# Optimization experiments

Hardware: AMD Instinct MI355X
Metric: run time of the kernel (lower is better)

Reference implementation:

```python
import jax, jax.numpy as jnp
import numpy as np

KSIZE, STRIDE, SCALE = 7, 4, 10.0


def _same_pad_amounts(n, k, s):
    out = -(-n // s)
    pad = max(0, (out - 1) * s + k - n)
    return pad // 2, pad - pad // 2, out


def _conv(x, w, b, stride=1, pad=0):
    y = jax.lax.conv_general_dilated(
        x, w, (stride, stride), [(pad, pad), (pad, pad)],
        dimension_numbers=("NCHW", "OIHW", "NCHW"))
    return y + b[None, :, None, None]


def setup_inputs() -> dict:
    key = jax.random.key(0)
    ks = jax.random.split(key, 10)
    B, Cin, H, W = 2, 64, 256, 256
    Ci = 16                       # inter_channels
    d_in = KSIZE * KSIZE * Ci     # 784 = ksize^2 * inter_channels
    d_out = d_in // 4             # 196
    s = 0.02
    return {
        "b": jax.random.normal(ks[0], (B, Cin, H, W), jnp.float32),
        "g_w": jax.random.normal(ks[1], (Ci, Cin, 3, 3), jnp.float32) * s,
        "g_b": jnp.zeros((Ci,), jnp.float32),
        "theta_w": jax.random.normal(ks[2], (Ci, Cin, 1, 1), jnp.float32) * s,
        "theta_b": jnp.zeros((Ci,), jnp.float32),
        "W_w": jax.random.normal(ks[3], (Cin, Ci, 1, 1), jnp.float32) * s,
        "W_b": jnp.zeros((Cin,), jnp.float32),
        "fc1_w": jax.random.normal(ks[4], (d_out, d_in), jnp.float32) * s,
        "fc1_b": jnp.zeros((d_out,), jnp.float32),
        "fc2_w": jax.random.normal(ks[5], (d_out, d_in), jnp.float32) * s,
        "fc2_b": jnp.zeros((d_out,), jnp.float32),
        "thr_w": jax.random.normal(ks[6], (1, Cin, KSIZE, KSIZE), jnp.float32) * s,
        "thr_b": jnp.zeros((1,), jnp.float32),
        "bias_w": jax.random.normal(ks[7], (1, Cin, KSIZE, KSIZE), jnp.float32) * s,
        "bias_b": jnp.zeros((1,), jnp.float32),
    }


def _forward(b, g_w, g_b, theta_w, theta_b, W_w, W_b, fc1_w, fc1_b,
             fc2_w, fc2_b, thr_w, thr_b, bias_w, bias_b):
    B, Cin, H, W = b.shape
    k, s = KSIZE, STRIDE
    pt, pb, Lh = _same_pad_amounts(H, k, s)
    pl, pr, Lw = _same_pad_amounts(W, k, s)
    L = Lh * Lw
    Ci = g_w.shape[0]

    b1 = _conv(b, g_w, g_b, 1, 1)            # [B,Ci,H,W]
    b2 = _conv(b, theta_w, theta_b, 1, 0)    # [B,Ci,H,W]
    b4 = jnp.pad(b, ((0, 0), (0, 0), (pt, pb), (pl, pr)))
    thr = _conv(b4, thr_w, thr_b, s, 0).reshape(B, L)   # per-patch threshold
    bias = _conv(b4, bias_w, bias_b, s, 0).reshape(B, L)  # per-patch bias

    # patch gather indices on the 'same'-padded grid (torch.Unfold order)
    R = (jnp.arange(Lh) * s)[:, None] + jnp.arange(k)[None, :]   # [Lh,k]
    Cc = (jnp.arange(Lw) * s)[:, None] + jnp.arange(k)[None, :]  # [Lw,k]
    Ri = R[:, None, :, None]                                     # -> [Lh,Lw,k,k]
    Cj = Cc[None, :, None, :]

    def patches(x):  # [B,Ci,H,W] -> [B,L,Ci*k*k], flatten order (C,kh,kw)
        xp = jnp.pad(x, ((0, 0), (0, 0), (pt, pb), (pl, pr)))
        p = xp[:, :, Ri, Cj]                       # [B,Ci,Lh,Lw,k,k]
        return p.transpose(0, 2, 3, 1, 4, 5).reshape(B, L, -1)

    wi = patches(b1)     # stride_1 patches of b1
    xi = wi              # b3 = b1 and stride_1 == stride_2 -> identical patches
    pi = patches(b2)     # stride_2 patches of b2, values to aggregate

    wi_f = jax.nn.relu(jnp.einsum("bld,od->blo", wi, fc1_w) + fc1_b)
    xi_f = jax.nn.relu(jnp.einsum("bld,od->blo", xi, fc2_w) + fc2_b)
    score = jnp.einsum("blo,bmo->blm", wi_f, xi_f)   # [B,L,L] patch similarity

    # threshold-gated sparse attention with learned per-patch thr/bias
    mask = (score >= thr[:, :, None]).astype(score.dtype)
    gated = score * mask + bias[:, :, None]
    attn = jax.nn.softmax(gated * SCALE, axis=-1) * mask
    attn = attn / (attn.sum(-1, keepdims=True) + 1e-8)

    agg = jnp.einsum("blm,bmd->bld", attn, pi)       # [B,L,Ci*k*k]
    p6 = agg.reshape(B, Lh, Lw, Ci, k, k).transpose(0, 3, 1, 2, 4, 5)

    # fold back (sum overlaps), normalize by overlap count, crop padding
    Hp, Wp = H + pt + pb, W + pl + pr
    folded = jnp.zeros((B, Ci, Hp, Wp), score.dtype).at[:, :, Ri, Cj].add(p6)
    cnt = jnp.zeros((Hp, Wp), score.dtype).at[Ri, Cj].add(1.0)
    zi = (folded / cnt)[:, :, pl:pl + H, pt:pt + W]

    return b + _conv(zi, W_w, W_b, 1, 0)


def reference(b, g_w, g_b, theta_w, theta_b, W_w, W_b, fc1_w, fc1_b,
              fc2_w, fc2_b, thr_w, thr_b, bias_w, bias_b):
    return _forward(b, g_w, g_b, theta_w, theta_b, W_w, W_b, fc1_w, fc1_b,
                    fc2_w, fc2_b, thr_w, thr_b, bias_w, bias_b)
```

## Files before the change

kernel.cpp:

```cpp
#include <hip/hip_runtime.h>
#include <math.h>

#define CIN  64
#define CI   16
#define HH   256
#define WWD  256
#define KS   7
#define STR  4
#define LH   64
#define LWD  64
#define LL   4096
#define DIN  784
#define DINP 896
#define DKP  832
#define DOUT 196
#define DOUTP 256
#define NB   2
#define YP   258
#define XP   264

typedef __attribute__((ext_vector_type(8))) short bf16x8;
typedef __attribute__((ext_vector_type(4))) float f32x4;
typedef __attribute__((ext_vector_type(16))) float f32x16;
typedef __attribute__((ext_vector_type(8))) int i32x8;
typedef __attribute__((ext_vector_type(4))) int i32x4;

__device__ __forceinline__ unsigned short f2bf(float x) {
    unsigned int u = __float_as_uint(x);
    unsigned int r = (u + 0x7FFFu + ((u >> 16) & 1u)) >> 16;
    return (unsigned short)r;
}
__device__ __forceinline__ float bf2f(unsigned short h) {
    return __uint_as_float(((unsigned int)h) << 16);
}

__device__ __forceinline__ void stage16(const void* g, void* l) {
#if defined(__has_builtin)
#if __has_builtin(__builtin_amdgcn_global_load_lds)
    __builtin_amdgcn_global_load_lds(
        (const __attribute__((address_space(1))) unsigned int*)g,
        (__attribute__((address_space(3))) unsigned int*)l, 16, 0, 0);
    return;
#endif
#endif
    *(float4*)l = *(const float4*)g;
}

__global__ __launch_bounds__(256) void k_prep_b(const float* __restrict__ b,
                                                unsigned short* __restrict__ bTp) {
    int blk = blockIdx.x;
    int s = blk & 7; int yy = (blk >> 3) % YP; int n = blk / (8 * YP);
    int y = yy - 1;
    for (int xx = threadIdx.x; xx < XP; xx += 256) {
        int x = xx - 4;
        bool v = (y >= 0 && y < 256 && x >= 0 && x < 256);
        unsigned short h[8];
#pragma unroll
        for (int j = 0; j < 8; j++)
            h[j] = v ? f2bf(b[((size_t)(n * 64 + s * 8 + j) * 256 + y) * 256 + x]) : (unsigned short)0;
        *(uint4*)&bTp[((((size_t)n * YP + yy) * 8 + s) * XP + xx) * 8] = *(uint4*)h;
    }
}

__global__ void k_prep_wb(const float* __restrict__ g_w, const float* __restrict__ th_w,
                          unsigned short* __restrict__ wbt) {
    int i = blockIdx.x * 256 + threadIdx.x;
    if (i >= 18432) return;
    int j = i & 7, co = (i >> 3) & 31, q = (i >> 8) & 3, h = (i >> 10) & 1, t = i >> 11;
    int ci = h * 32 + q * 8 + j;
    float v;
    if (co < 16) v = g_w[((size_t)co * 64 + ci) * 9 + t];
    else         v = (t == 4) ? th_w[(size_t)(co - 16) * 64 + ci] : 0.f;
    wbt[i] = f2bf(v);
}

__global__ void k_prep_fc(const float* __restrict__ fc1_w, const float* __restrict__ fc2_w,
                          unsigned short* __restrict__ fcwb) {
    int i = blockIdx.x * 256 + threadIdx.x;
    if (i >= 2 * DOUTP * DKP) return;
    int col = i % DKP; int row = (i / DKP) % DOUTP; int f = i / (DKP * DOUTP);
    float v = 0.f;
    if (row < DOUT && col < DIN) v = (f ? fc2_w : fc1_w)[row * DIN + col];
    fcwb[i] = f2bf(v);
}

__global__ __launch_bounds__(256) void k_convm(
        const unsigned short* __restrict__ bTp, const unsigned short* __restrict__ wbt,
        const float* __restrict__ g_b, const float* __restrict__ th_b,
        unsigned short* __restrict__ bx) {
    __shared__ unsigned short wb[18432];
    __shared__ unsigned short ti[8 * 3 * 68 * 8];
    int tid = threadIdx.x;
#pragma unroll
    for (int i = 0; i < 9; i++) {
        int c = i * 256 + tid;
        stage16(wbt + (size_t)c * 8, &wb[c * 8]);
    }
    int n = blockIdx.x >> 8, y = blockIdx.x & 255;
    int wave = tid >> 6, lane = tid & 63, lr = lane & 15, q = lane >> 4;
    int m0 = wave * 16;
    float bg = g_b[lr], bt = th_b[lr];
    for (int xs = 0; xs < 4; xs++) {
        __syncthreads();
        int x0 = xs * 64;
#pragma unroll
        for (int i = 0; i < 7; i++) {
            int c = i * 256 + tid;
            if (c < 1632) {
                int s = c / 204; int rem = c % 204; int r = rem / 68; int cc = rem % 68;
                const unsigned short* src =
                    bTp + ((((size_t)n * YP + y + r) * 8 + s) * XP + (x0 + 3 + cc)) * 8;
                stage16(src, &ti[c * 8]);
            }
        }
        __syncthreads();
        f32x4 a0 = {bg, bg, bg, bg}, a1 = {bt, bt, bt, bt};
#pragma unroll
        for (int t = 0; t < 9; t++) {
            int dy = t / 3, dx = t % 3;
#pragma unroll
            for (int h = 0; h < 2; h++) {
                int s = h * 4 + q;
                bf16x8 av = *(const bf16x8*)&ti[(((s * 3 + dy) * 68) + m0 + lr + dx) * 8];
                bf16x8 b0 = *(const bf16x8*)&wb[((((t * 2 + h) * 4 + q) * 32) + lr) * 8];
                bf16x8 b1 = *(const bf16x8*)&wb[((((t * 2 + h) * 4 + q) * 32) + 16 + lr) * 8];
                a0 = __builtin_amdgcn_mfma_f32_16x16x32_bf16(av, b0, a0, 0, 0, 0);
                a1 = __builtin_amdgcn_mfma_f32_16x16x32_bf16(av, b1, a1, 0, 0, 0);
            }
        }
        size_t pb = (((size_t)n * 256 + y) * 256 + x0 + m0 + q * 4);
#pragma unroll
        for (int r = 0; r < 4; r++) {
            bx[(pb + r) * 32 + lr]      = f2bf(a0[r]);
            bx[(pb + r) * 32 + 16 + lr] = f2bf(a1[r]);
        }
    }
}

__global__ __launch_bounds__(256) void k_thr(
        const unsigned short* __restrict__ bTp, const float* __restrict__ thr_w,
        const float* __restrict__ thr_b, float* __restrict__ thr) {
    __shared__ float w[64 * 49];
    int tid = threadIdx.x;
    for (int i = tid; i < 64 * 49; i += 256) w[i] = thr_w[i];
    __syncthreads();
    int wid = (blockIdx.x << 2) + (tid >> 6);
    int lane = tid & 63;
    int s = lane >> 3, j = lane & 7;
    int n = wid >> 12, l = wid & 4095;
    int lh = (l >> 6), lw = l & 63;
    const float* wl = w + (s * 8 + j) * 49;
    float acc = 0.f;
#pragma unroll
    for (int dy = 0; dy < 7; dy++) {
        int yy = lh * 4 + dy;
        if (yy >= YP) continue;
        const unsigned short* row = bTp + (((size_t)(n * YP + yy) * 8 + s) * XP) * 8;
#pragma unroll
        for (int dx = 0; dx < 7; dx++) {
            int xx = lw * 4 + dx + 3;
            acc = fmaf(bf2f(row[xx * 8 + j]), wl[dy * 7 + dx], acc);
        }
    }
#pragma unroll
    for (int off = 32; off > 0; off >>= 1) acc += __shfl_down(acc, off, 64);
    if (lane == 0) thr[wid] = acc + thr_b[0];
}

__global__ void k_patchesA(const unsigned short* __restrict__ bx, unsigned short* __restrict__ Pb) {
    size_t e = (size_t)blockIdx.x * 256 + threadIdx.x;
    if (e >= (size_t)NB * LL * DKP) return;
    int d = (int)(e % DKP); size_t r = e / DKP;
    int l = (int)(r & 4095); int n = (int)(r >> 12);
    unsigned short v = 0;
    if (d < DIN) {
        int ci = d / 49; int t = d % 49; int dy = t / 7; int dx = t % 7;
        int y = (l >> 6) * 4 + dy - 1, x = (l & 63) * 4 + dx - 1;
        if (y >= 0 && y < 256 && x >= 0 && x < 256)
            v = bx[(((size_t)n * 256 + y) * 256 + x) * 32 + ci];
    }
    Pb[e] = v;
}

__global__ void k_patchesT(const unsigned short* __restrict__ bx, unsigned char* __restrict__ piT8) {
    size_t e = (size_t)blockIdx.x * 256 + threadIdx.x;
    int l = (int)(e & 4095);
    int d = (int)((e >> 12) % DINP);
    int n = (int)(e / ((size_t)DINP * LL));
    float v = 0.f;
    if (d < DIN) {
        int ci = d / 49; int t = d % 49; int dy = t / 7; int dx = t % 7;
        int y = (l >> 6) * 4 + dy - 1, x = (l & 63) * 4 + dx - 1;
        if (y >= 0 && y < 256 && x >= 0 && x < 256)
            v = bf2f(bx[(((size_t)n * 256 + y) * 256 + x) * 32 + 16 + ci]);
    }
    int p = __builtin_amdgcn_cvt_pk_fp8_f32(v, 0.f, 0, false);
    piT8[e] = (unsigned char)(p & 0xFF);
}

template<int MODE>
__global__ __launch_bounds__(256) void k_gemm_nt(
        const unsigned short* __restrict__ A, const unsigned short* __restrict__ Bt,
        void* __restrict__ C, int lda, int ldb, int ldc, int K,
        size_t sA, size_t sB, size_t sC,
        const float* __restrict__ bias1, const float* __restrict__ bias2) {
    __shared__ unsigned short lA[2][128 * 64];
    __shared__ unsigned short lB[2][128 * 64];
    int tid = threadIdx.x;
    int wave = tid >> 6, lane = tid & 63;
    int lr = lane & 15, lq = lane >> 4;
    int wm = (wave >> 1) * 64, wn = (wave & 1) * 64;
    int i0 = blockIdx.x * 128, j0 = blockIdx.y * 128;
    int z = blockIdx.z;
    int az = (MODE == 2) ? (z >> 1) : z;
    int bz = (MODE == 2) ? (z & 1) : z;
    const unsigned short* Ab = A + (size_t)az * sA + (size_t)i0 * lda;
    const unsigned short* Bb = Bt + (size_t)bz * sB + (size_t)j0 * ldb;

    auto stageAB = [&](int buf, int k0) {
#pragma unroll
        for (int it = 0; it < 4; it++) {
            int c = it * 256 + tid;
            int row = c >> 3, slot = c & 7;
            int col8 = slot ^ (row & 7);
            stage16(Ab + (size_t)row * lda + k0 + col8 * 8, &lA[buf][c * 8]);
        }
#pragma unroll
        for (int it = 0; it < 4; it++) {
            int c = it * 256 + tid;
            int row = c >> 3, slot = c & 7;
            int col8 = slot ^ (row & 7);
            stage16(Bb + (size_t)row * ldb + k0 + col8 * 8, &lB[buf][c * 8]);
        }
    };

    f32x4 acc[4][4] = {};
    int NT = K >> 6;
    stageAB(0, 0);
    stageAB(1, 64);
    for (int t = 0; t < NT; ++t) {
        int cur = t & 1;
        if (t + 1 < NT) { asm volatile("s_waitcnt vmcnt(8)" ::: "memory"); }
        else            { asm volatile("s_waitcnt vmcnt(0)" ::: "memory"); }
        __builtin_amdgcn_s_barrier();
#pragma unroll
        for (int ks = 0; ks < 2; ks++) {
            bf16x8 af[4], bfr[4];
#pragma unroll
            for (int t2 = 0; t2 < 4; t2++) {
                int row = wm + t2 * 16 + lr;
                int slot = ks * 4 + lq;
                af[t2] = *(const bf16x8*)&lA[cur][row * 64 + (slot ^ (row & 7)) * 8];
            }
#pragma unroll
            for (int t2 = 0; t2 < 4; t2++) {
                int row = wn + t2 * 16 + lr;
                int slot = ks * 4 + lq;
                bfr[t2] = *(const bf16x8*)&lB[cur][row * 64 + (slot ^ (row & 7)) * 8];
            }
#pragma unroll
            for (int mi = 0; mi < 4; mi++)
#pragma unroll
                for (int nj = 0; nj < 4; nj++)
                    acc[mi][nj] = __builtin_amdgcn_mfma_f32_16x16x32_bf16(
                        af[mi], bfr[nj], acc[mi][nj], 0, 0, 0);
        }
        asm volatile("s_waitcnt lgkmcnt(0)" ::: "memory");
        __builtin_amdgcn_s_barrier();
        if (t + 2 < NT) stageAB(cur, (t + 2) << 6);
    }
    if (MODE == 1) {
        unsigned short* Cb = (unsigned short*)C + (size_t)z * sC;
#pragma unroll
        for (int mi = 0; mi < 4; mi++)
#pragma unroll
            for (int r = 0; r < 4; r++) {
                int row = i0 + wm + mi * 16 + lq * 4 + r;
#pragma unroll
                for (int nj = 0; nj < 4; nj++)
                    Cb[(size_t)row * ldc + j0 + wn + nj * 16 + lr] = f2bf(acc[mi][nj][r]);
            }
    } else {
        const float* biasp = bz ? bias2 : bias1;
        unsigned short* Cb = (unsigned short*)C + (size_t)z * sC;
#pragma unroll
        for (int mi = 0; mi < 4; mi++)
#pragma unroll
            for (int r = 0; r < 4; r++) {
                int row = i0 + wm + mi * 16 + lq * 4 + r;
#pragma unroll
                for (int nj = 0; nj < 4; nj++) {
                    int col = j0 + wn + nj * 16 + lr;
                    float bv = (col < DOUT) ? biasp[col] : 0.f;
                    float v = fmaxf(acc[mi][nj][r] + bv, 0.f);
                    Cb[(size_t)row * ldc + col] = f2bf(v);
                }
            }
    }
}

__global__ __launch_bounds__(256) void k_gemm_mx(
        const unsigned char* __restrict__ A, const unsigned char* __restrict__ Bt,
        unsigned short* __restrict__ C, int lda, int ldb, int ldc, int K,
        size_t sA, size_t sB, size_t sC) {
    __shared__ unsigned char lA[2][128 * 128];
    __shared__ unsigned char lB[2][128 * 128];
    int tid = threadIdx.x;
    int wave = tid >> 6, lane = tid & 63;
    int lr = lane & 31, hf = lane >> 5;
    int wm = (wave >> 1) * 64, wn = (wave & 1) * 64;
    int i0 = blockIdx.x * 128, j0 = blockIdx.y * 128;
    int z = blockIdx.z;
    const unsigned char* Ab = A + (size_t)z * sA + (size_t)i0 * lda;
    const unsigned char* Bb = Bt + (size_t)z * sB + (size_t)j0 * ldb;

    auto stageAB = [&](int buf, int k0) {
#pragma unroll
        for (int it = 0; it < 4; it++) {
            int c = it * 256 + tid;
            int row = c >> 3, slot = c & 7;
            int col16 = slot ^ ((row ^ (row >> 3)) & 7);
            stage16(Ab + (size_t)row * lda + k0 + col16 * 16, &lA[buf][c * 16]);
        }
#pragma unroll
        for (int it = 0; it < 4; it++) {
            int c = it * 256 + tid;
            int row = c >> 3, slot = c & 7;
            int col16 = slot ^ ((row ^ (row >> 3)) & 7);
            stage16(Bb + (size_t)row * ldb + k0 + col16 * 16, &lB[buf][c * 16]);
        }
    };

    f32x16 acc[2][2] = {};
    int NT = K >> 7;
    stageAB(0, 0);
    stageAB(1, 128);
    for (int t = 0; t < NT; ++t) {
        int cur = t & 1;
        if (t + 1 < NT) { asm volatile("s_waitcnt vmcnt(8)" ::: "memory"); }
        else           { asm volatile("s_waitcnt vmcnt(0)" ::: "memory"); }
        __builtin_amdgcn_s_barrier();
        asm volatile("" ::: "memory");
#pragma unroll
        for (int kk = 0; kk < 2; kk++) {
            i32x8 af[2], bfv[2];
            int c0 = kk * 4 + hf * 2;
#pragma unroll
            for (int t2 = 0; t2 < 2; t2++) {
                int row = wm + t2 * 32 + lr;
                int sw = (row ^ (row >> 3)) & 7;
                i32x4 lo = *(const i32x4*)&lA[cur][row * 128 + ((c0    ) ^ sw) * 16];
                i32x4 hi = *(const i32x4*)&lA[cur][row * 128 + ((c0 + 1) ^ sw) * 16];
                af[t2][0] = lo[0]; af[t2][1] = lo[1]; af[t2][2] = lo[2]; af[t2][3] = lo[3];
                af[t2][4] = hi[0]; af[t2][5] = hi[1]; af[t2][6] = hi[2]; af[t2][7] = hi[3];
            }
#pragma unroll
            for (int t2 = 0; t2 < 2; t2++) {
                int row = wn + t2 * 32 + lr;
                int sw = (row ^ (row >> 3)) & 7;
                i32x4 lo = *(const i32x4*)&lB[cur][row * 128 + ((c0    ) ^ sw) * 16];
                i32x4 hi = *(const i32x4*)&lB[cur][row * 128 + ((c0 + 1) ^ sw) * 16];
                bfv[t2][0] = lo[0]; bfv[t2][1] = lo[1]; bfv[t2][2] = lo[2]; bfv[t2][3] = lo[3];
                bfv[t2][4] = hi[0]; bfv[t2][5] = hi[1]; bfv[t2][6] = hi[2]; bfv[t2][7] = hi[3];
            }
#pragma unroll
            for (int mi = 0; mi < 2; mi++)
#pragma unroll
                for (int nj = 0; nj < 2; nj++)
                    acc[mi][nj] = __builtin_amdgcn_mfma_scale_f32_32x32x64_f8f6f4(
                        af[mi], bfv[nj], acc[mi][nj],
                        0, 0,
                        0, 0x7F7F7F7F,
                        0, 0x7F7F7F7F);
        }
        asm volatile("s_waitcnt lgkmcnt(0)" ::: "memory");
        __builtin_amdgcn_s_barrier();
        if (t + 2 < NT) stageAB(cur, (t + 2) << 7);
    }
    unsigned short* Cb = C + (size_t)z * sC;
#pragma unroll
    for (int mi = 0; mi < 2; mi++)
#pragma unroll
        for (int nj = 0; nj < 2; nj++)
#pragma unroll
            for (int reg = 0; reg < 16; reg++) {
                int row = i0 + wm + mi * 32 + (reg & 3) + 8 * (reg >> 2) + 4 * hf;
                int col = j0 + wn + nj * 32 + lr;
                Cb[(size_t)row * ldc + col] = f2bf(acc[mi][nj][reg]);
            }
}

__global__ __launch_bounds__(256) void k_softmax(
        const unsigned short* __restrict__ score, const float* __restrict__ thr,
        unsigned char* __restrict__ attn8) {
    __shared__ float red[256], red2[256];
    int row = blockIdx.x, tid = threadIdx.x;
    const uint4* g4 = (const uint4*)(score + (size_t)row * LL);
    float t = thr[row];
    uint4 u0 = g4[tid], u1 = g4[tid + 256];
    float v[16];
    {
        unsigned int w[8] = {u0.x, u0.y, u0.z, u0.w, u1.x, u1.y, u1.z, u1.w};
#pragma unroll
        for (int q = 0; q < 8; q++) {
            v[2 * q]     = __uint_as_float(w[q] << 16);
            v[2 * q + 1] = __uint_as_float(w[q] & 0xFFFF0000u);
        }
    }
    float mx = 0.f;
#pragma unroll
    for (int k = 0; k < 16; k++) if (v[k] >= t) mx = fmaxf(mx, v[k]);
    red[tid] = mx; __syncthreads();
    for (int st = 128; st > 0; st >>= 1) {
        if (tid < st) red[tid] = fmaxf(red[tid], red[tid + st]);
        __syncthreads();
    }
    float M = 10.f * fmaxf(red[0], 0.f);
    __syncthreads();
    float e[16];
    float s2 = 0.f, n0 = 0.f;
#pragma unroll
    for (int k = 0; k < 16; k++) {
        if (v[k] >= t) { e[k] = __expf(10.f * v[k] - M); s2 += e[k]; }
        else           { e[k] = 0.f; n0 += 1.f; }
    }
    red[tid] = s2; red2[tid] = n0; __syncthreads();
    for (int st = 128; st > 0; st >>= 1) {
        if (tid < st) { red[tid] += red[tid + st]; red2[tid] += red2[tid + st]; }
        __syncthreads();
    }
    float S2 = red[0], N0 = red2[0];
    float iD = 1.f / (S2 + 1e-8f * (S2 + N0 * __expf(-M)));
#pragma unroll
    for (int i = 0; i < 2; i++) {
        int c = tid + i * 256;
        int d0 = __builtin_amdgcn_cvt_pk_fp8_f32(e[i * 8 + 0] * iD, e[i * 8 + 1] * iD, 0, false);
        d0     = __builtin_amdgcn_cvt_pk_fp8_f32(e[i * 8 + 2] * iD, e[i * 8 + 3] * iD, d0, true);
        int d1 = __builtin_amdgcn_cvt_pk_fp8_f32(e[i * 8 + 4] * iD, e[i * 8 + 5] * iD, 0, false);
        d1     = __builtin_amdgcn_cvt_pk_fp8_f32(e[i * 8 + 6] * iD, e[i * 8 + 7] * iD, d1, true);
        *(uint2*)&attn8[(size_t)row * LL + (size_t)c * 8] = make_uint2((unsigned)d0, (unsigned)d1);
    }
}

__global__ void k_fold(const unsigned short* __restrict__ aggb, float* __restrict__ zi) {
    int p = blockIdx.x * 256 + threadIdx.x;
    int x = p & 255, y = (p >> 8) & 255, ci = (p >> 16) & 15, n = p >> 20;
    int yp = y + 1, xp = x + 1;
    int lh1 = yp >> 2; if (lh1 > 63) lh1 = 63;
    int lh0 = (yp >= 3) ? ((yp - 3) >> 2) : 0;
    int lw1 = xp >> 2; if (lw1 > 63) lw1 = 63;
    int lw0 = (xp >= 3) ? ((xp - 3) >> 2) : 0;
    const unsigned short* a0 = aggb + (size_t)n * LL * DINP;
    float sum = 0.f;
    for (int lh = lh0; lh <= lh1; lh++) {
        int dy = yp - 4 * lh;
        for (int lw = lw0; lw <= lw1; lw++) {
            int dx = xp - 4 * lw;
            sum += bf2f(a0[(size_t)(lh * 64 + lw) * DINP + ci * 49 + dy * 7 + dx]);
        }
    }
    float cnt = (float)((lh1 - lh0 + 1) * (lw1 - lw0 + 1));
    zi[p] = sum / cnt;
}

__global__ void k_final(const float* __restrict__ zi, const float* __restrict__ b,
                        const float* __restrict__ W_w, const float* __restrict__ W_b,
                        float* __restrict__ out) {
    __shared__ float w[16 * 64];
    int tid = threadIdx.x;
    for (int i = tid; i < 16 * 64; i += 256) {
        int ci = i >> 6; int co = i & 63;
        w[i] = W_w[co * 16 + ci];
    }
    __syncthreads();
    int p = blockIdx.x * 256 + tid;
    int n = p >> 16, yx = p & 65535;
    float acc[64];
#pragma unroll
    for (int co = 0; co < 64; co++) acc[co] = 0.f;
    const float* zn = zi + (size_t)n * 16 * 65536;
#pragma unroll
    for (int ci = 0; ci < 16; ci++) {
        float v = zn[ci * 65536 + yx];
#pragma unroll
        for (int co = 0; co < 64; co++) acc[co] += v * w[ci * 64 + co];
    }
    const float* bn = b + (size_t)n * 64 * 65536;
    float* on = out + (size_t)n * 64 * 65536;
#pragma unroll
    for (int co = 0; co < 64; co++) on[co * 65536 + yx] = bn[co * 65536 + yx] + acc[co] + W_b[co];
}

extern "C" void kernel_launch(void* const* d_in, const int* in_sizes, int n_in,
                              void* d_out, int out_size, void* d_ws, size_t ws_size,
                              hipStream_t stream) {
    const float* b     = (const float*)d_in[0];
    const float* g_w   = (const float*)d_in[1];
    const float* g_b   = (const float*)d_in[2];
    const float* th_w  = (const float*)d_in[3];
    const float* th_b  = (const float*)d_in[4];
    const float* W_w   = (const float*)d_in[5];
    const float* W_b   = (const float*)d_in[6];
    const float* fc1_w = (const float*)d_in[7];
    const float* fc1_b = (const float*)d_in[8];
    const float* fc2_w = (const float*)d_in[9];
    const float* fc2_b = (const float*)d_in[10];
    const float* thr_w = (const float*)d_in[11];
    const float* thr_b = (const float*)d_in[12];
    float* out = (float*)d_out;

    float* ws = (float*)d_ws;
    size_t off = 0;
    auto alloc = [&](size_t nf) { float* p = ws + off; off += (nf + 63) & ~(size_t)63; return p; };
    unsigned short* aggb = (unsigned short*)alloc((size_t)NB * LL * DINP / 2);
    float* zi   = alloc((size_t)NB * CI * HH * WWD);
    unsigned short* bTp  = (unsigned short*)alloc((size_t)NB * YP * 8 * XP * 8 / 2);
    unsigned short* bx   = (unsigned short*)alloc((size_t)NB * HH * WWD * 32 / 2);
    unsigned short* Pb   = (unsigned short*)alloc((size_t)NB * LL * DKP / 2);
    unsigned char*  piT8 = (unsigned char*)alloc((size_t)NB * DINP * LL / 4);
    unsigned short* fcout = (unsigned short*)alloc((size_t)NB * 2 * LL * DOUTP / 2);
    unsigned short* wbt  = (unsigned short*)alloc(18432 / 2);
    unsigned short* fcwb = (unsigned short*)alloc((size_t)2 * DOUTP * DKP / 2);
    float* thr  = alloc((size_t)NB * LL);
    unsigned short* score = (unsigned short*)alloc((size_t)NB * LL * LL / 2);
    unsigned char*  attn8 = (unsigned char*)alloc((size_t)NB * LL * LL / 4);

    k_prep_b<<<dim3(NB * YP * 8), 256, 0, stream>>>(b, bTp);
    k_prep_wb<<<dim3(72), 256, 0, stream>>>(g_w, th_w, wbt);
    k_prep_fc<<<dim3((2 * DOUTP * DKP + 255) / 256), 256, 0, stream>>>(fc1_w, fc2_w, fcwb);
    k_convm<<<dim3(NB * 256), 256, 0, stream>>>(bTp, wbt, g_b, th_b, bx);
    k_thr<<<dim3(2048), 256, 0, stream>>>(bTp, thr_w, thr_b, thr);
    k_patchesA<<<dim3((int)((size_t)NB * LL * DKP / 256)), 256, 0, stream>>>(bx, Pb);
    k_patchesT<<<dim3((int)((size_t)NB * DINP * LL / 256)), 256, 0, stream>>>(bx, piT8);
    k_gemm_nt<2><<<dim3(32, 2, 4), 256, 0, stream>>>(
        Pb, fcwb, (void*)fcout, DKP, DKP, DOUTP, DKP,
        (size_t)LL * DKP, (size_t)DOUTP * DKP, (size_t)LL * DOUTP, fc1_b, fc2_b);
    k_gemm_nt<1><<<dim3(32, 32, NB), 256, 0, stream>>>(
        fcout, fcout + (size_t)LL * DOUTP, (void*)score, DOUTP, DOUTP, LL, DOUTP,
        (size_t)2 * LL * DOUTP, (size_t)2 * LL * DOUTP, (size_t)LL * LL, nullptr, nullptr);
    k_softmax<<<dim3(NB * LL), 256, 0, stream>>>(score, thr, attn8);
    k_gemm_mx<<<dim3(32, DINP / 128, NB), 256, 0, stream>>>(
        attn8, piT8, aggb, LL, LL, DINP, LL,
        (size_t)LL * LL, (size_t)DINP * LL, (size_t)LL * DINP);
    k_fold<<<dim3(8192), 256, 0, stream>>>(aggb, zi);
    k_final<<<dim3(512), 256, 0, stream>>>(zi, b, W_w, W_b, out);
}
```

Before: 323.0 us.

## Fuse patch extraction into one LDS-staged kernel and XCD-swizzle GEMM grids

Merges the two element-wise patch-extraction kernels into one kernel. It stages a 7x68 pixel tile of the conv output in shared memory and writes both the bf16 patch matrix and the transposed fp8 patch matrix with 16-byte vector stores. This removes redundant scattered global gathers and byte-wide stores. Separately, the GEMM launches become 1D grids remapped so that consecutive tiles land on the same XCD (stride-8 interleave), aiming for better L2 reuse across chiplets. The remap assumes the block count is divisible by 8.

```diff
diff --git a/kernel.cpp b/kernel.cpp
--- a/kernel.cpp
+++ b/kernel.cpp
@@ -46,6 +46,13 @@
     *(float4*)l = *(const float4*)g;
 }
 
+__device__ __forceinline__ void swz_grid(int gx, int gy, int& ib, int& jb, int& zb) {
+    int total = gridDim.x;
+    int flat = blockIdx.x;
+    int s = (flat & 7) * (total >> 3) + (flat >> 3);
+    ib = s % gx; int rem = s / gx; jb = rem % gy; zb = rem / gy;
+}
+
 __global__ __launch_bounds__(256) void k_prep_b(const float* __restrict__ b,
                                                 unsigned short* __restrict__ bTp) {
     int blk = blockIdx.x;
@@ -167,35 +174,67 @@
     if (lane == 0) thr[wid] = acc + thr_b[0];
 }
 
-__global__ void k_patchesA(const unsigned short* __restrict__ bx, unsigned short* __restrict__ Pb) {
-    size_t e = (size_t)blockIdx.x * 256 + threadIdx.x;
-    if (e >= (size_t)NB * LL * DKP) return;
-    int d = (int)(e % DKP); size_t r = e / DKP;
-    int l = (int)(r & 4095); int n = (int)(r >> 12);
-    unsigned short v = 0;
-    if (d < DIN) {
-        int ci = d / 49; int t = d % 49; int dy = t / 7; int dx = t % 7;
-        int y = (l >> 6) * 4 + dy - 1, x = (l & 63) * 4 + dx - 1;
-        if (y >= 0 && y < 256 && x >= 0 && x < 256)
-            v = bx[(((size_t)n * 256 + y) * 256 + x) * 32 + ci];
-    }
-    Pb[e] = v;
-}
-
-__global__ void k_patchesT(const unsigned short* __restrict__ bx, unsigned char* __restrict__ piT8) {
-    size_t e = (size_t)blockIdx.x * 256 + threadIdx.x;
-    int l = (int)(e & 4095);
-    int d = (int)((e >> 12) % DINP);
-    int n = (int)(e / ((size_t)DINP * LL));
-    float v = 0.f;
-    if (d < DIN) {
-        int ci = d / 49; int t = d % 49; int dy = t / 7; int dx = t % 7;
-        int y = (l >> 6) * 4 + dy - 1, x = (l & 63) * 4 + dx - 1;
-        if (y >= 0 && y < 256 && x >= 0 && x < 256)
-            v = bf2f(bx[(((size_t)n * 256 + y) * 256 + x) * 32 + 16 + ci]);
-    }
-    int p = __builtin_amdgcn_cvt_pk_fp8_f32(v, 0.f, 0, false);
-    piT8[e] = (unsigned char)(p & 0xFF);
+__global__ __launch_bounds__(256) void k_patches(
+        const unsigned short* __restrict__ bx,
+        unsigned short* __restrict__ Pb, unsigned char* __restrict__ piT8) {
+    __shared__ unsigned short sh[7][68][32];
+    int tid = threadIdx.x;
+    int blk = blockIdx.x;
+    int lwg = blk & 3, lh = (blk >> 2) & 63, n = blk >> 8;
+    int x0 = lwg * 64 - 1;
+    int y0 = lh * 4 - 1;
+    for (int it = 0; it < 8; it++) {
+        int c = it * 256 + tid;
+        if (c < 1904) {
+            int q = c & 3, xx = (c >> 2) % 68, r = c / 272;
+            int y = y0 + r, x = x0 + xx;
+            uint4 v = make_uint4(0u, 0u, 0u, 0u);
+            if (y >= 0 && y < 256 && x >= 0 && x < 256)
+                v = *(const uint4*)&bx[(((size_t)(n * 256 + y) * 256 + x) * 32) + q * 8];
+            *(uint4*)&sh[r][xx][q * 8] = v;
+        }
+    }
+    __syncthreads();
+    for (int it = 0; it < 7; it++) {
+        int idx = it * 256 + tid;
+        if (idx < 16 * 104) {
+            int lwl = idx / 104, v8 = idx % 104;
+            unsigned short o[8];
+#pragma unroll
+            for (int k = 0; k < 8; k++) {
+                int d = v8 * 8 + k;
+                unsigned short val = 0;
+                if (d < DIN) {
+                    int ci = d / 49, t = d % 49, dy = t / 7, dx = t % 7;
+                    val = sh[dy][lwl * 4 + dx][ci];
+                }
+                o[k] = val;
+            }
+            int l = lh * 64 + lwg * 16 + lwl;
+            *(uint4*)&Pb[((size_t)n * LL + l) * DKP + v8 * 8] = *(uint4*)o;
+        }
+    }
+    for (int it = 0; it < 4; it++) {
+        int d = it * 256 + tid;
+        if (d < DINP) {
+            unsigned int w[4] = {0u, 0u, 0u, 0u};
+            if (d < DIN) {
+                int ci = d / 49, t = d % 49, dy = t / 7, dx = t % 7;
+#pragma unroll
+                for (int p = 0; p < 4; p++) {
+                    float v0 = bf2f(sh[dy][(p * 4 + 0) * 4 + dx][16 + ci]);
+                    float v1 = bf2f(sh[dy][(p * 4 + 1) * 4 + dx][16 + ci]);
+                    float v2 = bf2f(sh[dy][(p * 4 + 2) * 4 + dx][16 + ci]);
+                    float v3 = bf2f(sh[dy][(p * 4 + 3) * 4 + dx][16 + ci]);
+                    int a = __builtin_amdgcn_cvt_pk_fp8_f32(v0, v1, 0, false);
+                    a     = __builtin_amdgcn_cvt_pk_fp8_f32(v2, v3, a, true);
+                    w[p] = (unsigned)a;
+                }
+            }
+            *(uint4*)&piT8[((size_t)n * DINP + d) * LL + lh * 64 + lwg * 16] =
+                make_uint4(w[0], w[1], w[2], w[3]);
+        }
+    }
 }
 
 template<int MODE>
@@ -203,15 +242,17 @@
         const unsigned short* __restrict__ A, const unsigned short* __restrict__ Bt,
         void* __restrict__ C, int lda, int ldb, int ldc, int K,
         size_t sA, size_t sB, size_t sC,
-        const float* __restrict__ bias1, const float* __restrict__ bias2) {
+        const float* __restrict__ bias1, const float* __restrict__ bias2,
+        int gx, int gy) {
     __shared__ unsigned short lA[2][128 * 64];
     __shared__ unsigned short lB[2][128 * 64];
     int tid = threadIdx.x;
     int wave = tid >> 6, lane = tid & 63;
     int lr = lane & 15, lq = lane >> 4;
     int wm = (wave >> 1) * 64, wn = (wave & 1) * 64;
-    int i0 = blockIdx.x * 128, j0 = blockIdx.y * 128;
-    int z = blockIdx.z;
+    int ib, jb, z;
+    swz_grid(gx, gy, ib, jb, z);
+    int i0 = ib * 128, j0 = jb * 128;
     int az = (MODE == 2) ? (z >> 1) : z;
     int bz = (MODE == 2) ? (z & 1) : z;
     const unsigned short* Ab = A + (size_t)az * sA + (size_t)i0 * lda;
@@ -302,15 +343,16 @@
 __global__ __launch_bounds__(256) void k_gemm_mx(
         const unsigned char* __restrict__ A, const unsigned char* __restrict__ Bt,
         unsigned short* __restrict__ C, int lda, int ldb, int ldc, int K,
-        size_t sA, size_t sB, size_t sC) {
+        size_t sA, size_t sB, size_t sC, int gx, int gy) {
     __shared__ unsigned char lA[2][128 * 128];
     __shared__ unsigned char lB[2][128 * 128];
     int tid = threadIdx.x;
     int wave = tid >> 6, lane = tid & 63;
     int lr = lane & 31, hf = lane >> 5;
     int wm = (wave >> 1) * 64, wn = (wave & 1) * 64;
-    int i0 = blockIdx.x * 128, j0 = blockIdx.y * 128;
-    int z = blockIdx.z;
+    int ib, jb, z;
+    swz_grid(gx, gy, ib, jb, z);
+    int i0 = ib * 128, j0 = jb * 128;
     const unsigned char* Ab = A + (size_t)z * sA + (size_t)i0 * lda;
     const unsigned char* Bb = Bt + (size_t)z * sB + (size_t)j0 * ldb;
 
@@ -530,18 +572,17 @@
     k_prep_fc<<<dim3((2 * DOUTP * DKP + 255) / 256), 256, 0, stream>>>(fc1_w, fc2_w, fcwb);
     k_convm<<<dim3(NB * 256), 256, 0, stream>>>(bTp, wbt, g_b, th_b, bx);
     k_thr<<<dim3(2048), 256, 0, stream>>>(bTp, thr_w, thr_b, thr);
-    k_patchesA<<<dim3((int)((size_t)NB * LL * DKP / 256)), 256, 0, stream>>>(bx, Pb);
-    k_patchesT<<<dim3((int)((size_t)NB * DINP * LL / 256)), 256, 0, stream>>>(bx, piT8);
-    k_gemm_nt<2><<<dim3(32, 2, 4), 256, 0, stream>>>(
+    k_patches<<<dim3(NB * 64 * 4), 256, 0, stream>>>(bx, Pb, piT8);
+    k_gemm_nt<2><<<dim3(256), 256, 0, stream>>>(
         Pb, fcwb, (void*)fcout, DKP, DKP, DOUTP, DKP,
-        (size_t)LL * DKP, (size_t)DOUTP * DKP, (size_t)LL * DOUTP, fc1_b, fc2_b);
-    k_gemm_nt<1><<<dim3(32, 32, NB), 256, 0, stream>>>(
+        (size_t)LL * DKP, (size_t)DOUTP * DKP, (size_t)LL * DOUTP, fc1_b, fc2_b, 32, 2);
+    k_gemm_nt<1><<<dim3(2048), 256, 0, stream>>>(
         fcout, fcout + (size_t)LL * DOUTP, (void*)score, DOUTP, DOUTP, LL, DOUTP,
-        (size_t)2 * LL * DOUTP, (size_t)2 * LL * DOUTP, (size_t)LL * LL, nullptr, nullptr);
+        (size_t)2 * LL * DOUTP, (size_t)2 * LL * DOUTP, (size_t)LL * LL, nullptr, nullptr, 32, 32);
     k_softmax<<<dim3(NB * LL), 256, 0, stream>>>(score, thr, attn8);
-    k_gemm_mx<<<dim3(32, DINP / 128, NB), 256, 0, stream>>>(
+    k_gemm_mx<<<dim3(448), 256, 0, stream>>>(
         attn8, piT8, aggb, LL, LL, DINP, LL,
-        (size_t)LL * LL, (size_t)DINP * LL, (size_t)LL * DINP);
+        (size_t)LL * LL, (size_t)DINP * LL, (size_t)LL * DINP, 32, 7);
     k_fold<<<dim3(8192), 256, 0, stream>>>(aggb, zi);
     k_final<<<dim3(512), 256, 0, stream>>>(zi, b, W_w, W_b, out);
 }
```

After: 299.8 us. 7.2% less time.
